# Kernel optimization log

Measured on AMD Instinct MI355X. Metric: run time of the kernel, lower is better.

## Reference

```python
import jax, jax.numpy as jnp
import numpy as np

H = 128  # hidden size

def _lstm_layer(x, Wih, Whh, bih, bhh):
    # x: [B, T, D]; Wih: [4H, D]; Whh: [4H, H]; biases: [4H]
    B, T, _ = x.shape
    # Precompute input contribution for all timesteps (one big GEMM)
    xg = jnp.einsum('btd,gd->btg', x, Wih) + bih + bhh  # [B, T, 4H]
    xg = jnp.swapaxes(xg, 0, 1)  # time-major [T, B, 4H]

    def step(carry, xt):
        h, c = carry
        gates = xt + h @ Whh.T  # [B, 4H]
        i, f, g, o = jnp.split(gates, 4, axis=-1)
        i = jax.nn.sigmoid(i)
        f = jax.nn.sigmoid(f)
        g = jnp.tanh(g)
        o = jax.nn.sigmoid(o)
        c = f * c + i * g
        h = o * jnp.tanh(c)
        return (h, c), h

    h0 = jnp.zeros((B, H), dtype=x.dtype)
    c0 = jnp.zeros((B, H), dtype=x.dtype)
    (_, _), hs = jax.lax.scan(step, (h0, c0), xg)
    return jnp.swapaxes(hs, 0, 1)  # [B, T, H]


def setup_inputs() -> dict:
    key = jax.random.key(0)
    ks = jax.random.split(key, 9)
    B, T, D = 32, 2048, 64
    s0 = 1.0 / np.sqrt(H)
    x = jax.random.normal(ks[0], (B, T, D), dtype=jnp.float32)
    # layer 0: input dim 64, layer 1: input dim 128 (torch gate order i,f,g,o)
    Wih0 = jax.random.uniform(ks[1], (4 * H, D), jnp.float32, -s0, s0)
    Whh0 = jax.random.uniform(ks[2], (4 * H, H), jnp.float32, -s0, s0)
    bih0 = jax.random.uniform(ks[3], (4 * H,), jnp.float32, -s0, s0)
    bhh0 = jax.random.uniform(ks[4], (4 * H,), jnp.float32, -s0, s0)
    Wih1 = jax.random.uniform(ks[5], (4 * H, H), jnp.float32, -s0, s0)
    Whh1 = jax.random.uniform(ks[6], (4 * H, H), jnp.float32, -s0, s0)
    bih1 = jax.random.uniform(ks[7], (4 * H,), jnp.float32, -s0, s0)
    bhh1 = jax.random.uniform(ks[8], (4 * H,), jnp.float32, -s0, s0)
    return {"x": x, "Wih0": Wih0, "Whh0": Whh0, "bih0": bih0, "bhh0": bhh0,
            "Wih1": Wih1, "Whh1": Whh1, "bih1": bih1, "bhh1": bhh1}


def reference(x, Wih0, Whh0, bih0, bhh0, Wih1, Whh1, bih1, bhh1):
    h = _lstm_layer(x, Wih0, Whh0, bih0, bhh0)
    h = _lstm_layer(h, Wih1, Whh1, bih1, bhh1)
    return h  # [B, T, H] full hidden-state sequence of the top layer
```

## Files before the change

### kernel.cpp

```cpp
#include <hip/hip_runtime.h>

#define TLEN 2048
#define BATCH 32
#define DIN 64
#define HID 128
#define RING 256
#define CHK 8

typedef _Float16 h2 __attribute__((ext_vector_type(2)));
typedef float f4 __attribute__((ext_vector_type(4)));
typedef unsigned int u32;

#if defined(__has_builtin)
#if __has_builtin(__builtin_amdgcn_fdot2)
#define FDOT2(a, b, c) __builtin_amdgcn_fdot2((a), (b), (c), false)
#endif
#endif
#ifndef FDOT2
#define FDOT2(a, b, c) ((c) + (float)(a).x * (float)(b).x + (float)(a).y * (float)(b).y)
#endif
#define DOT2U(wu, hv, acc) FDOT2(__builtin_bit_cast(h2, (wu)), (hv), (acc))

__device__ __forceinline__ float sigm(float x) { return 1.0f / (1.0f + __expf(-x)); }
__device__ __forceinline__ float tanh_c(float x) {
    x = fminf(fmaxf(x, -15.0f), 15.0f);
    float e = __expf(2.0f * x);
    return (e - 1.0f) / (e + 1.0f);
}
__device__ __forceinline__ void qreduce(float (&v)[4]) {
    #pragma unroll
    for (int m = 0; m < 4; ++m) {
        v[m] += __shfl_xor(v[m], 1, 4);
        v[m] += __shfl_xor(v[m], 2, 4);
    }
}

__device__ __forceinline__ u32 aload_rlx(u32* p) {
    return __hip_atomic_load(p, __ATOMIC_RELAXED, __HIP_MEMORY_SCOPE_AGENT);
}
__device__ __forceinline__ u32 aload_acq(u32* p) {
    return __hip_atomic_load(p, __ATOMIC_ACQUIRE, __HIP_MEMORY_SCOPE_AGENT);
}
__device__ __forceinline__ void astore_rlx(u32* p, u32 v) {
    __hip_atomic_store(p, v, __ATOMIC_RELAXED, __HIP_MEMORY_SCOPE_AGENT);
}
__device__ __forceinline__ void astore_rel(u32* p, u32 v) {
    __hip_atomic_store(p, v, __ATOMIC_RELEASE, __HIP_MEMORY_SCOPE_AGENT);
}

__device__ __forceinline__ void load_w_slice(const float* __restrict__ W,
                                             int rg, int kg, u32 (&w)[64]) {
    #pragma unroll
    for (int m = 0; m < 4; ++m) {
        const float2* a = (const float2*)(W + (size_t)(rg + 128 * m) * HID + kg * 32);
        #pragma unroll
        for (int i = 0; i < 16; ++i) {
            float2 v = a[i];
            h2 x; x.x = (_Float16)v.x; x.y = (_Float16)v.y;
            w[m * 16 + i] = __builtin_bit_cast(u32, x);
        }
    }
    #pragma unroll
    for (int i = 0; i < 64; ++i) asm volatile("" : "+v"(w[i]));
}
__device__ __forceinline__ void dot_slice(const u32 (&w)[64],
                                          const uint4* __restrict__ H,
                                          float (&p)[4]) {
    #pragma unroll
    for (int qr = 0; qr < 4; ++qr) {
        u32 hw[4];
        *(uint4*)hw = H[qr];
        #pragma unroll
        for (int ww = 0; ww < 4; ++ww) {
            const h2 hv = __builtin_bit_cast(h2, hw[ww]);
            #pragma unroll
            for (int m = 0; m < 4; ++m)
                p[m] = DOT2U(w[m * 16 + qr * 4 + ww], hv, p[m]);
        }
    }
}

__global__ __launch_bounds__(512) void xg_precompute(
    const float* __restrict__ X, const float* __restrict__ Wih0,
    const float* __restrict__ bih0, const float* __restrict__ bhh0,
    _Float16* __restrict__ XG)
{
    __shared__ float xs[16][DIN];
    const int blk = blockIdx.x;
    const int b   = blk / (TLEN / 16);
    const int tc  = blk % (TLEN / 16);
    const int j   = threadIdx.x;
    const int row = (j >> 2) + 128 * (j & 3);

    const float* xsrc = X + ((size_t)b * TLEN + (size_t)tc * 16) * DIN;
    for (int i = j; i < 16 * DIN; i += 512) ((float*)xs)[i] = xsrc[i];
    __syncthreads();

    f4 w[16];
    const f4* wp = (const f4*)(Wih0 + (size_t)row * DIN);
    #pragma unroll
    for (int i = 0; i < 16; ++i) w[i] = wp[i];
    const float bias = bih0[row] + bhh0[row];

    _Float16* dst = XG + ((size_t)b * TLEN + (size_t)tc * 16) * 512 + j;
    #pragma unroll 4
    for (int t = 0; t < 16; ++t) {
        float acc = bias;
        const f4* xv = (const f4*)&xs[t][0];
        #pragma unroll
        for (int i = 0; i < 16; ++i) {
            f4 x4 = xv[i];
            acc += w[i][0] * x4[0] + w[i][1] * x4[1] + w[i][2] * x4[2] + w[i][3] * x4[3];
        }
        dst[(size_t)t * 512] = (_Float16)acc;
    }
}

__global__ __launch_bounds__(512, 2) void lstm2_pipe(
    const _Float16* __restrict__ XG0,
    const float* __restrict__ Whh0,
    const float* __restrict__ Wih1, const float* __restrict__ Whh1,
    const float* __restrict__ bih1, const float* __restrict__ bhh1,
    float* __restrict__ Out,
    u32* __restrict__ H0g,
    u32* __restrict__ XG1,
    u32* __restrict__ Flags)
{
    const int role = blockIdx.x / BATCH;
    const int b    = blockIdx.x % BATCH;
    const int t0   = threadIdx.x;
    const int rg   = t0 >> 2;
    const int kg   = t0 & 3;

    u32* F0 = Flags + (size_t)b * 16;
    u32* F1 = Flags + (size_t)(32 + b) * 16;
    u32* C2 = Flags + (size_t)(64 + b) * 16;

    if (role == 0) {
        __shared__ alignas(16) _Float16 hl[2][HID];
        u32 w[64];
        load_w_slice(Whh0, rg, kg, w);
        if (t0 < HID) { hl[0][t0] = (_Float16)0.0f; hl[1][t0] = (_Float16)0.0f; }
        float c0 = 0.0f;
        const _Float16* xgp = XG0 + (size_t)b * TLEN * 512 + t0;
        u32* h0out = H0g + (size_t)b * TLEN * 64;
        _Float16 xga = xgp[0];
        _Float16 xgb = xgp[512];
        __syncthreads();

        for (int t = 0; t < TLEN; ++t) {
            const int cur = t & 1, prv = cur ^ 1;
            const float xgv = (float)xga;
            xga = xgb;
            { int tn = (t + 2 < TLEN) ? t + 2 : TLEN - 1; xgb = xgp[(size_t)tn * 512]; }

            float p[4];
            #pragma unroll
            for (int m = 0; m < 4; ++m) p[m] = (kg == m) ? xgv : 0.0f;
            dot_slice(w, (const uint4*)&hl[prv][kg * 32], p);
            qreduce(p);
            float ii = sigm(p[0]), ff = sigm(p[1]);
            float gg = tanh_c(p[2]), oo = sigm(p[3]);
            c0 = ff * c0 + ii * gg;
            if (kg == 0) hl[cur][rg] = (_Float16)(oo * tanh_c(c0));
            __syncthreads();
            if (t0 < 64)
                astore_rlx(&h0out[(size_t)t * 64 + t0], ((const u32*)hl[cur])[t0]);
            if (t0 == 0 && (t & (CHK - 1)) == (CHK - 1))
                astore_rel(F0, (u32)(t + 1));
        }
    } else if (role == 1) {
        __shared__ alignas(16) u32 h0c[CHK * 64];
        u32 w[64];
        load_w_slice(Wih1, rg, kg, w);
        const int rowk = rg + 128 * kg;
        const float B1 = bih1[rowk] + bhh1[rowk];
        u32* H0in = H0g + (size_t)b * TLEN * 64;
        u32* xout = XG1 + (size_t)b * RING * 512;
        u32 sc = 0;
        __syncthreads();

        for (int c = 0; c < TLEN / CHK; ++c) {
            const int tbase = c * CHK;
            if (t0 == 0) {
                u32 av; long g = 0;
                do { av = aload_acq(F0);
                     if (av >= (u32)(tbase + CHK)) break;
                     __builtin_amdgcn_s_sleep(2);
                } while (++g < 50000000L);
                if (tbase + CHK > (int)sc + (RING - 64)) {
                    g = 0;
                    do { sc = aload_rlx(C2);
                         if (tbase + CHK <= (int)sc + (RING - 64)) break;
                         __builtin_amdgcn_s_sleep(2);
                    } while (++g < 50000000L);
                }
            }
            __syncthreads();
            h0c[t0] = aload_rlx(&H0in[(size_t)tbase * 64 + t0]);
            __syncthreads();

            #pragma unroll
            for (int s = 0; s < CHK; ++s) {
                const int t = tbase + s;
                float p[4];
                #pragma unroll
                for (int m = 0; m < 4; ++m) p[m] = (kg == m) ? B1 : 0.0f;
                dot_slice(w, (const uint4*)&h0c[s * 64 + kg * 16], p);
                qreduce(p);
                astore_rlx(&xout[(size_t)((t & (RING - 1))) * 512 + t0],
                           __builtin_bit_cast(u32, p[kg]));
            }
            asm volatile("s_waitcnt vmcnt(0)" ::: "memory");
            __syncthreads();
            if (t0 == 0) astore_rel(F1, (u32)(tbase + CHK));
        }
    } else {
        __shared__ alignas(16) _Float16 hl[2][HID];
        __shared__ alignas(16) u32 xgc[CHK * 512];
        u32 w[64];
        load_w_slice(Whh1, rg, kg, w);
        if (t0 < HID) { hl[0][t0] = (_Float16)0.0f; hl[1][t0] = (_Float16)0.0f; }
        u32* xin = XG1 + (size_t)b * RING * 512;
        float c1 = 0.0f;
        __syncthreads();

        for (int c = 0; c < TLEN / CHK; ++c) {
            const int tbase = c * CHK;
            if (t0 == 0) {
                u32 av; long g = 0;
                do { av = aload_acq(F1);
                     if (av >= (u32)(tbase + CHK)) break;
                     __builtin_amdgcn_s_sleep(2);
                } while (++g < 50000000L);
            }
            __syncthreads();
            const size_t rbase = (size_t)(tbase & (RING - 1)) * 512;
            #pragma unroll
            for (int k = 0; k < CHK; ++k)
                xgc[k * 512 + t0] = aload_rlx(&xin[rbase + k * 512 + t0]);
            __syncthreads();

            #pragma unroll 1
            for (int s = 0; s < CHK; ++s) {
                const int t = tbase + s;
                const int cur = t & 1, prv = cur ^ 1;
                const float xgv = __builtin_bit_cast(float, xgc[s * 512 + t0]);

                float q[4];
                #pragma unroll
                for (int m = 0; m < 4; ++m) q[m] = (kg == m) ? xgv : 0.0f;
                dot_slice(w, (const uint4*)&hl[prv][kg * 32], q);
                qreduce(q);
                float ii = sigm(q[0]), ff = sigm(q[1]);
                float gg = tanh_c(q[2]), oo = sigm(q[3]);
                c1 = ff * c1 + ii * gg;
                float h1v = oo * tanh_c(c1);
                if (kg == 0) {
                    hl[cur][rg] = (_Float16)h1v;
                    Out[((size_t)b * TLEN + t) * HID + rg] = h1v;
                }
                __syncthreads();
            }
            if (t0 == 0 && (c & 3) == 3)
                astore_rlx(C2, (u32)(tbase + CHK));
        }
    }
}

__global__ __launch_bounds__(512, 2) void lstm2_persist(
    const float* __restrict__ X,
    const float* __restrict__ Wih0, const float* __restrict__ Whh0,
    const float* __restrict__ bih0, const float* __restrict__ bhh0,
    const float* __restrict__ Wih1, const float* __restrict__ Whh1,
    const float* __restrict__ bih1, const float* __restrict__ bhh1,
    float* __restrict__ Out)
{
    __shared__ unsigned int wih0_lds[512 * 33];
    __shared__ _Float16 h0buf[2][HID];
    __shared__ _Float16 h1buf[2][HID];

    const int b  = blockIdx.x;
    const int t  = threadIdx.x;
    const int rg = t >> 2;
    const int kg = t & 3;

    {
        const float2* src = (const float2*)(Wih0 + t * DIN);
        #pragma unroll
        for (int i = 0; i < 32; ++i) {
            float2 v = src[i];
            h2 p; p.x = (_Float16)v.x; p.y = (_Float16)v.y;
            wih0_lds[t * 33 + i] = __builtin_bit_cast(unsigned int, p);
        }
    }
    if (t < HID) {
        h0buf[0][t] = (_Float16)0.0f; h0buf[1][t] = (_Float16)0.0f;
        h1buf[0][t] = (_Float16)0.0f; h1buf[1][t] = (_Float16)0.0f;
    }

    h2 whh0[4][16], wih1[4][16], whh1[4][16];
    float bi0[4], bi1[4];
    #pragma unroll
    for (int m = 0; m < 4; ++m) {
        const int row = rg + 128 * m;
        const float2* a = (const float2*)(Whh0 + row * HID + kg * 32);
        const float2* c = (const float2*)(Wih1 + row * HID + kg * 32);
        const float2* d = (const float2*)(Whh1 + row * HID + kg * 32);
        #pragma unroll
        for (int i = 0; i < 16; ++i) {
            float2 v; h2 w;
            v = a[i]; w.x = (_Float16)v.x; w.y = (_Float16)v.y; whh0[m][i] = w;
            v = c[i]; w.x = (_Float16)v.x; w.y = (_Float16)v.y; wih1[m][i] = w;
            v = d[i]; w.x = (_Float16)v.x; w.y = (_Float16)v.y; whh1[m][i] = w;
        }
        bi0[m] = (kg == 0) ? (bih0[row] + bhh0[row]) : 0.0f;
        bi1[m] = (kg == 0) ? (bih1[row] + bhh1[row]) : 0.0f;
    }

    float c0 = 0.0f, c1 = 0.0f;
    __syncthreads();

    f4 xA[4], xB[4];
    {
        const f4* xp = (const f4*)(X + ((size_t)b * TLEN) * DIN + kg * 16);
        #pragma unroll
        for (int j = 0; j < 4; ++j) xA[j] = xp[j];
    }

    auto step = [&](int tt, f4 (&xc)[4], f4 (&xn)[4]) {
        const int cur = tt & 1, nxt = cur ^ 1;
        h2 xh[8];
        const float* xf = (const float*)xc;
        #pragma unroll
        for (int j = 0; j < 8; ++j) {
            h2 p; p.x = (_Float16)xf[2 * j]; p.y = (_Float16)xf[2 * j + 1];
            xh[j] = p;
        }
        {
            const int tn = (tt + 1 < TLEN) ? tt + 1 : TLEN - 1;
            const f4* xp = (const f4*)(X + ((size_t)b * TLEN + tn) * DIN + kg * 16);
            #pragma unroll
            for (int j = 0; j < 4; ++j) xn[j] = xp[j];
        }
        float p0[4];
        #pragma unroll
        for (int m = 0; m < 4; ++m) p0[m] = bi0[m];
        #pragma unroll
        for (int m = 0; m < 4; ++m) {
            const unsigned int* wr = &wih0_lds[(rg + 128 * m) * 33 + kg * 8];
            #pragma unroll
            for (int i = 0; i < 8; ++i) {
                h2 w = __builtin_bit_cast(h2, wr[i]);
                p0[m] = FDOT2(w, xh[i], p0[m]);
            }
        }
        {
            const unsigned int* hr = (const unsigned int*)&h0buf[cur][0];
            #pragma unroll
            for (int i = 0; i < 16; ++i) {
                h2 hv = __builtin_bit_cast(h2, hr[kg * 16 + i]);
                #pragma unroll
                for (int m = 0; m < 4; ++m)
                    p0[m] = FDOT2(whh0[m][i], hv, p0[m]);
            }
        }
        #pragma unroll
        for (int m = 0; m < 4; ++m) {
            p0[m] += __shfl_xor(p0[m], 1, 4);
            p0[m] += __shfl_xor(p0[m], 2, 4);
        }
        {
            float ii = sigm(p0[0]), ff = sigm(p0[1]);
            float gg = tanh_c(p0[2]), oo = sigm(p0[3]);
            c0 = ff * c0 + ii * gg;
            float h0v = oo * tanh_c(c0);
            if (kg == 0) h0buf[nxt][rg] = (_Float16)h0v;
        }
        __syncthreads();
        float q[4];
        #pragma unroll
        for (int m = 0; m < 4; ++m) q[m] = bi1[m];
        {
            const unsigned int* hr = (const unsigned int*)&h0buf[nxt][0];
            #pragma unroll
            for (int i = 0; i < 16; ++i) {
                h2 hv = __builtin_bit_cast(h2, hr[kg * 16 + i]);
                #pragma unroll
                for (int m = 0; m < 4; ++m)
                    q[m] = FDOT2(wih1[m][i], hv, q[m]);
            }
        }
        {
            const unsigned int* hr = (const unsigned int*)&h1buf[cur][0];
            #pragma unroll
            for (int i = 0; i < 16; ++i) {
                h2 hv = __builtin_bit_cast(h2, hr[kg * 16 + i]);
                #pragma unroll
                for (int m = 0; m < 4; ++m)
                    q[m] = FDOT2(whh1[m][i], hv, q[m]);
            }
        }
        #pragma unroll
        for (int m = 0; m < 4; ++m) {
            q[m] += __shfl_xor(q[m], 1, 4);
            q[m] += __shfl_xor(q[m], 2, 4);
        }
        {
            float ii = sigm(q[0]), ff = sigm(q[1]);
            float gg = tanh_c(q[2]), oo = sigm(q[3]);
            c1 = ff * c1 + ii * gg;
            float h1v = oo * tanh_c(c1);
            if (kg == 0) {
                h1buf[nxt][rg] = (_Float16)h1v;
                Out[((size_t)b * TLEN + tt) * HID + rg] = h1v;
            }
        }
        __syncthreads();
    };

    for (int tt = 0; tt < TLEN; tt += 2) {
        step(tt, xA, xB);
        step(tt + 1, xB, xA);
    }
}

extern "C" void kernel_launch(void* const* d_in, const int* in_sizes, int n_in,
                              void* d_out, int out_size, void* d_ws, size_t ws_size,
                              hipStream_t stream) {
    const float* X    = (const float*)d_in[0];
    const float* Wih0 = (const float*)d_in[1];
    const float* Whh0 = (const float*)d_in[2];
    const float* bih0 = (const float*)d_in[3];
    const float* bhh0 = (const float*)d_in[4];
    const float* Wih1 = (const float*)d_in[5];
    const float* Whh1 = (const float*)d_in[6];
    const float* bih1 = (const float*)d_in[7];
    const float* bhh1 = (const float*)d_in[8];
    float* Out = (float*)d_out;

    const size_t XG0_B  = (size_t)BATCH * TLEN * 512 * 2;
    const size_t H0_B   = (size_t)BATCH * TLEN * 64 * 4;
    const size_t XG1_B  = (size_t)BATCH * RING * 512 * 4;
    const size_t FLAG_B = 96 * 16 * 4;
    const size_t NEED   = XG0_B + H0_B + XG1_B + FLAG_B;

    if (ws_size >= NEED) {
        char* ws = (char*)d_ws;
        _Float16* XG0 = (_Float16*)ws;
        u32* H0g   = (u32*)(ws + XG0_B);
        u32* XG1   = (u32*)(ws + XG0_B + H0_B);
        u32* Flags = (u32*)(ws + XG0_B + H0_B + XG1_B);

        hipMemsetAsync(Flags, 0, FLAG_B, stream);
        xg_precompute<<<dim3(BATCH * (TLEN / 16)), dim3(512), 0, stream>>>(
            X, Wih0, bih0, bhh0, XG0);
        lstm2_pipe<<<dim3(3 * BATCH), dim3(512), 0, stream>>>(
            XG0, Whh0, Wih1, Whh1, bih1, bhh1, Out, H0g, XG1, Flags);
    } else {
        lstm2_persist<<<dim3(BATCH), dim3(512), 0, stream>>>(
            X, Wih0, Whh0, bih0, bhh0, Wih1, Whh1, bih1, bhh1, Out);
    }
}
```

Baseline: 2.338 ms.

## Split LSTM recurrence dot products across eight lanes with 1024-thread blocks

The pipelined two-layer LSTM kernel now runs 1024 threads per block instead of 512. Each gate row's 128-wide dot product is split across eight lanes instead of four, so each thread holds half as many fp16 weight registers and does half as many fdot2 operations per timestep. The aim is to shorten the per-step serial latency of the recurrence. In exchange it adds a third shuffle-reduction stage, has redundant lanes (only four of the eight lanes carry gate values), and makes each per-step barrier span twice as many waves.

New measurement: 2.921 ms. 24.9% more time.

```diff
diff --git a/kernel.cpp b/kernel.cpp
--- a/kernel.cpp
+++ b/kernel.cpp
@@ -27,11 +27,12 @@
     float e = __expf(2.0f * x);
     return (e - 1.0f) / (e + 1.0f);
 }
-__device__ __forceinline__ void qreduce(float (&v)[4]) {
+__device__ __forceinline__ void qreduce8(float (&v)[4]) {
     #pragma unroll
     for (int m = 0; m < 4; ++m) {
-        v[m] += __shfl_xor(v[m], 1, 4);
-        v[m] += __shfl_xor(v[m], 2, 4);
+        v[m] += __shfl_xor(v[m], 1, 8);
+        v[m] += __shfl_xor(v[m], 2, 8);
+        v[m] += __shfl_xor(v[m], 4, 8);
     }
 }
 
@@ -48,26 +49,26 @@
     __hip_atomic_store(p, v, __ATOMIC_RELEASE, __HIP_MEMORY_SCOPE_AGENT);
 }
 
-__device__ __forceinline__ void load_w_slice(const float* __restrict__ W,
-                                             int rg, int kg, u32 (&w)[64]) {
+__device__ __forceinline__ void load_w8(const float* __restrict__ W,
+                                        int rg, int kg, u32 (&w)[32]) {
     #pragma unroll
     for (int m = 0; m < 4; ++m) {
-        const float2* a = (const float2*)(W + (size_t)(rg + 128 * m) * HID + kg * 32);
-        #pragma unroll
-        for (int i = 0; i < 16; ++i) {
+        const float2* a = (const float2*)(W + (size_t)(rg + 128 * m) * HID + kg * 16);
+        #pragma unroll
+        for (int i = 0; i < 8; ++i) {
             float2 v = a[i];
             h2 x; x.x = (_Float16)v.x; x.y = (_Float16)v.y;
-            w[m * 16 + i] = __builtin_bit_cast(u32, x);
-        }
-    }
-    #pragma unroll
-    for (int i = 0; i < 64; ++i) asm volatile("" : "+v"(w[i]));
-}
-__device__ __forceinline__ void dot_slice(const u32 (&w)[64],
-                                          const uint4* __restrict__ H,
-                                          float (&p)[4]) {
-    #pragma unroll
-    for (int qr = 0; qr < 4; ++qr) {
+            w[m * 8 + i] = __builtin_bit_cast(u32, x);
+        }
+    }
+    #pragma unroll
+    for (int i = 0; i < 32; ++i) asm volatile("" : "+v"(w[i]));
+}
+__device__ __forceinline__ void dot8(const u32 (&w)[32],
+                                     const uint4* __restrict__ H,
+                                     float (&p)[4]) {
+    #pragma unroll
+    for (int qr = 0; qr < 2; ++qr) {
         u32 hw[4];
         *(uint4*)hw = H[qr];
         #pragma unroll
@@ -75,7 +76,7 @@
             const h2 hv = __builtin_bit_cast(h2, hw[ww]);
             #pragma unroll
             for (int m = 0; m < 4; ++m)
-                p[m] = DOT2U(w[m * 16 + qr * 4 + ww], hv, p[m]);
+                p[m] = DOT2U(w[m * 8 + qr * 4 + ww], hv, p[m]);
         }
     }
 }
@@ -116,7 +117,7 @@
     }
 }
 
-__global__ __launch_bounds__(512, 2) void lstm2_pipe(
+__global__ __launch_bounds__(1024, 1) void lstm2_pipe(
     const _Float16* __restrict__ XG0,
     const float* __restrict__ Whh0,
     const float* __restrict__ Wih1, const float* __restrict__ Whh1,
@@ -129,8 +130,9 @@
     const int role = blockIdx.x / BATCH;
     const int b    = blockIdx.x % BATCH;
     const int t0   = threadIdx.x;
-    const int rg   = t0 >> 2;
-    const int kg   = t0 & 3;
+    const int rg   = t0 >> 3;
+    const int kg   = t0 & 7;
+    const int g    = kg & 3;
 
     u32* F0 = Flags + (size_t)b * 16;
     u32* F1 = Flags + (size_t)(32 + b) * 16;
@@ -138,11 +140,11 @@
 
     if (role == 0) {
         __shared__ alignas(16) _Float16 hl[2][HID];
-        u32 w[64];
-        load_w_slice(Whh0, rg, kg, w);
+        u32 w[32];
+        load_w8(Whh0, rg, kg, w);
         if (t0 < HID) { hl[0][t0] = (_Float16)0.0f; hl[1][t0] = (_Float16)0.0f; }
         float c0 = 0.0f;
-        const _Float16* xgp = XG0 + (size_t)b * TLEN * 512 + t0;
+        const _Float16* xgp = XG0 + (size_t)b * TLEN * 512 + rg * 4 + g;
         u32* h0out = H0g + (size_t)b * TLEN * 64;
         _Float16 xga = xgp[0];
         _Float16 xgb = xgp[512];
@@ -157,8 +159,8 @@
             float p[4];
             #pragma unroll
             for (int m = 0; m < 4; ++m) p[m] = (kg == m) ? xgv : 0.0f;
-            dot_slice(w, (const uint4*)&hl[prv][kg * 32], p);
-            qreduce(p);
+            dot8(w, (const uint4*)&hl[prv][kg * 16], p);
+            qreduce8(p);
             float ii = sigm(p[0]), ff = sigm(p[1]);
             float gg = tanh_c(p[2]), oo = sigm(p[3]);
             c0 = ff * c0 + ii * gg;
@@ -171,9 +173,9 @@
         }
     } else if (role == 1) {
         __shared__ alignas(16) u32 h0c[CHK * 64];
-        u32 w[64];
-        load_w_slice(Wih1, rg, kg, w);
-        const int rowk = rg + 128 * kg;
+        u32 w[32];
+        load_w8(Wih1, rg, kg, w);
+        const int rowk = rg + 128 * g;
         const float B1 = bih1[rowk] + bhh1[rowk];
         u32* H0in = H0g + (size_t)b * TLEN * 64;
         u32* xout = XG1 + (size_t)b * RING * 512;
@@ -183,21 +185,22 @@
         for (int c = 0; c < TLEN / CHK; ++c) {
             const int tbase = c * CHK;
             if (t0 == 0) {
-                u32 av; long g = 0;
+                u32 av; long gd = 0;
                 do { av = aload_acq(F0);
                      if (av >= (u32)(tbase + CHK)) break;
                      __builtin_amdgcn_s_sleep(2);
-                } while (++g < 50000000L);
+                } while (++gd < 50000000L);
                 if (tbase + CHK > (int)sc + (RING - 64)) {
-                    g = 0;
+                    gd = 0;
                     do { sc = aload_rlx(C2);
                          if (tbase + CHK <= (int)sc + (RING - 64)) break;
                          __builtin_amdgcn_s_sleep(2);
-                    } while (++g < 50000000L);
+                    } while (++gd < 50000000L);
                 }
             }
             __syncthreads();
-            h0c[t0] = aload_rlx(&H0in[(size_t)tbase * 64 + t0]);
+            if (t0 < CHK * 64)
+                h0c[t0] = aload_rlx(&H0in[(size_t)tbase * 64 + t0]);
             __syncthreads();
 
             #pragma unroll
@@ -206,10 +209,11 @@
                 float p[4];
                 #pragma unroll
                 for (int m = 0; m < 4; ++m) p[m] = (kg == m) ? B1 : 0.0f;
-                dot_slice(w, (const uint4*)&h0c[s * 64 + kg * 16], p);
-                qreduce(p);
-                astore_rlx(&xout[(size_t)((t & (RING - 1))) * 512 + t0],
-                           __builtin_bit_cast(u32, p[kg]));
+                dot8(w, (const uint4*)&h0c[s * 64 + kg * 8], p);
+                qreduce8(p);
+                if (kg < 4)
+                    astore_rlx(&xout[(size_t)(t & (RING - 1)) * 512 + rg * 4 + kg],
+                               __builtin_bit_cast(u32, p[kg]));
             }
             asm volatile("s_waitcnt vmcnt(0)" ::: "memory");
             __syncthreads();
@@ -218,8 +222,8 @@
     } else {
         __shared__ alignas(16) _Float16 hl[2][HID];
         __shared__ alignas(16) u32 xgc[CHK * 512];
-        u32 w[64];
-        load_w_slice(Whh1, rg, kg, w);
+        u32 w[32];
+        load_w8(Whh1, rg, kg, w);
         if (t0 < HID) { hl[0][t0] = (_Float16)0.0f; hl[1][t0] = (_Float16)0.0f; }
         u32* xin = XG1 + (size_t)b * RING * 512;
         float c1 = 0.0f;
@@ -228,30 +232,31 @@
         for (int c = 0; c < TLEN / CHK; ++c) {
             const int tbase = c * CHK;
             if (t0 == 0) {
-                u32 av; long g = 0;
+                u32 av; long gd = 0;
                 do { av = aload_acq(F1);
                      if (av >= (u32)(tbase + CHK)) break;
                      __builtin_amdgcn_s_sleep(2);
-                } while (++g < 50000000L);
+                } while (++gd < 50000000L);
             }
             __syncthreads();
             const size_t rbase = (size_t)(tbase & (RING - 1)) * 512;
             #pragma unroll
-            for (int k = 0; k < CHK; ++k)
-                xgc[k * 512 + t0] = aload_rlx(&xin[rbase + k * 512 + t0]);
+            for (int k = 0; k < (CHK * 512) / 1024; ++k)
+                xgc[k * 1024 + t0] = aload_rlx(&xin[rbase + k * 1024 + t0]);
             __syncthreads();
 
             #pragma unroll 1
             for (int s = 0; s < CHK; ++s) {
                 const int t = tbase + s;
                 const int cur = t & 1, prv = cur ^ 1;
-                const float xgv = __builtin_bit_cast(float, xgc[s * 512 + t0]);
+                const float xgv = __builtin_bit_cast(float,
+                                    xgc[s * 512 + rg * 4 + g]);
 
                 float q[4];
                 #pragma unroll
                 for (int m = 0; m < 4; ++m) q[m] = (kg == m) ? xgv : 0.0f;
-                dot_slice(w, (const uint4*)&hl[prv][kg * 32], q);
-                qreduce(q);
+                dot8(w, (const uint4*)&hl[prv][kg * 16], q);
+                qreduce8(q);
                 float ii = sigm(q[0]), ff = sigm(q[1]);
                 float gg = tanh_c(q[2]), oo = sigm(q[3]);
                 c1 = ff * c1 + ii * gg;
@@ -455,7 +460,7 @@
         hipMemsetAsync(Flags, 0, FLAG_B, stream);
         xg_precompute<<<dim3(BATCH * (TLEN / 16)), dim3(512), 0, stream>>>(
             X, Wih0, bih0, bhh0, XG0);
-        lstm2_pipe<<<dim3(3 * BATCH), dim3(512), 0, stream>>>(
+        lstm2_pipe<<<dim3(3 * BATCH), dim3(1024), 0, stream>>>(
             XG0, Whh0, Wih1, Whh1, bih1, bhh1, Out, H0g, XG1, Flags);
     } else {
         lstm2_persist<<<dim3(BATCH), dim3(512), 0, stream>>>(
```

## Stage recurrent weights in LDS and use exp2/rcp gate activations

Applied to the files above, without the earlier changes.

Each role of the pipelined LSTM kernel now converts its 512x128 weight matrix to fp16 once and stores it in a padded shared-memory pool. The matvec reads weights from there every step instead of keeping a 64-register slice per thread, and the launch bound no longer asks for two blocks per CU. The aim is to cut register pressure and possible spills. The trade-off is extra LDS reads on the serial critical path of every timestep. Sigmoid and tanh are rewritten with the hardware exp2 and reciprocal builtins to shorten the activation latency.

Measured after the change: 2.160 ms. 1.08x faster.

```diff
diff --git a/kernel.cpp b/kernel.cpp
--- a/kernel.cpp
+++ b/kernel.cpp
@@ -6,7 +6,9 @@
 #define HID 128
 #define RING 256
 #define CHK 8
-
+#define WRS 68
+
+typedef _Float16 f16;
 typedef _Float16 h2 __attribute__((ext_vector_type(2)));
 typedef float f4 __attribute__((ext_vector_type(4)));
 typedef unsigned int u32;
@@ -21,11 +23,28 @@
 #endif
 #define DOT2U(wu, hv, acc) FDOT2(__builtin_bit_cast(h2, (wu)), (hv), (acc))
 
-__device__ __forceinline__ float sigm(float x) { return 1.0f / (1.0f + __expf(-x)); }
+#if defined(__has_builtin)
+#if __has_builtin(__builtin_amdgcn_exp2f)
+#define FEXP2(x) __builtin_amdgcn_exp2f(x)
+#endif
+#if __has_builtin(__builtin_amdgcn_rcpf)
+#define FRCP(x) __builtin_amdgcn_rcpf(x)
+#endif
+#endif
+#ifndef FEXP2
+#define FEXP2(x) __expf((x) * 0.69314718f)
+#endif
+#ifndef FRCP
+#define FRCP(x) (1.0f / (x))
+#endif
+
+__device__ __forceinline__ float sigm(float x) {
+    return FRCP(1.0f + FEXP2(-1.44269504f * x));
+}
 __device__ __forceinline__ float tanh_c(float x) {
     x = fminf(fmaxf(x, -15.0f), 15.0f);
-    float e = __expf(2.0f * x);
-    return (e - 1.0f) / (e + 1.0f);
+    float e = FEXP2(2.88539008f * x);
+    return (e - 1.0f) * FRCP(e + 1.0f);
 }
 __device__ __forceinline__ void qreduce(float (&v)[4]) {
     #pragma unroll
@@ -35,10 +54,10 @@
     }
 }
 
-__device__ __forceinline__ u32 aload_rlx(u32* p) {
+__device__ __forceinline__ u32 aload_rlx(const u32* p) {
     return __hip_atomic_load(p, __ATOMIC_RELAXED, __HIP_MEMORY_SCOPE_AGENT);
 }
-__device__ __forceinline__ u32 aload_acq(u32* p) {
+__device__ __forceinline__ u32 aload_acq(const u32* p) {
     return __hip_atomic_load(p, __ATOMIC_ACQUIRE, __HIP_MEMORY_SCOPE_AGENT);
 }
 __device__ __forceinline__ void astore_rlx(u32* p, u32 v) {
@@ -48,34 +67,35 @@
     __hip_atomic_store(p, v, __ATOMIC_RELEASE, __HIP_MEMORY_SCOPE_AGENT);
 }
 
-__device__ __forceinline__ void load_w_slice(const float* __restrict__ W,
-                                             int rg, int kg, u32 (&w)[64]) {
+__device__ __forceinline__ void stage_weights(const float* __restrict__ W,
+                                              u32* __restrict__ wl, int t0) {
+    const float2* src2 = (const float2*)W;
+    for (int idx = t0; idx < 512 * 64; idx += 512) {
+        const int row = idx >> 6, d = idx & 63;
+        float2 v = src2[(size_t)row * 64 + d];
+        h2 x; x.x = (f16)v.x; x.y = (f16)v.y;
+        wl[(size_t)row * WRS + d] = __builtin_bit_cast(u32, x);
+    }
+}
+
+__device__ __forceinline__ void dot_wlds(const u32* __restrict__ wl,
+                                         int rg, int kg,
+                                         const u32* __restrict__ hsl,
+                                         float (&p)[4]) {
+    uint4 hq[4];
+    #pragma unroll
+    for (int i4 = 0; i4 < 4; ++i4) hq[i4] = *(const uint4*)&hsl[i4 * 4];
     #pragma unroll
     for (int m = 0; m < 4; ++m) {
-        const float2* a = (const float2*)(W + (size_t)(rg + 128 * m) * HID + kg * 32);
-        #pragma unroll
-        for (int i = 0; i < 16; ++i) {
-            float2 v = a[i];
-            h2 x; x.x = (_Float16)v.x; x.y = (_Float16)v.y;
-            w[m * 16 + i] = __builtin_bit_cast(u32, x);
-        }
-    }
-    #pragma unroll
-    for (int i = 0; i < 64; ++i) asm volatile("" : "+v"(w[i]));
-}
-__device__ __forceinline__ void dot_slice(const u32 (&w)[64],
-                                          const uint4* __restrict__ H,
-                                          float (&p)[4]) {
-    #pragma unroll
-    for (int qr = 0; qr < 4; ++qr) {
-        u32 hw[4];
-        *(uint4*)hw = H[qr];
-        #pragma unroll
-        for (int ww = 0; ww < 4; ++ww) {
-            const h2 hv = __builtin_bit_cast(h2, hw[ww]);
-            #pragma unroll
-            for (int m = 0; m < 4; ++m)
-                p[m] = DOT2U(w[m * 16 + qr * 4 + ww], hv, p[m]);
+        const u32* wb = wl + (size_t)(rg + 128 * m) * WRS + kg * 16;
+        #pragma unroll
+        for (int i4 = 0; i4 < 4; ++i4) {
+            const uint4 wq = *(const uint4*)&wb[i4 * 4];
+            const u32* hw = (const u32*)&hq[i4];
+            p[m] = DOT2U(wq.x, __builtin_bit_cast(h2, hw[0]), p[m]);
+            p[m] = DOT2U(wq.y, __builtin_bit_cast(h2, hw[1]), p[m]);
+            p[m] = DOT2U(wq.z, __builtin_bit_cast(h2, hw[2]), p[m]);
+            p[m] = DOT2U(wq.w, __builtin_bit_cast(h2, hw[3]), p[m]);
         }
     }
 }
@@ -83,7 +103,7 @@
 __global__ __launch_bounds__(512) void xg_precompute(
     const float* __restrict__ X, const float* __restrict__ Wih0,
     const float* __restrict__ bih0, const float* __restrict__ bhh0,
-    _Float16* __restrict__ XG)
+    f16* __restrict__ XG)
 {
     __shared__ float xs[16][DIN];
     const int blk = blockIdx.x;
@@ -102,7 +122,7 @@
     for (int i = 0; i < 16; ++i) w[i] = wp[i];
     const float bias = bih0[row] + bhh0[row];
 
-    _Float16* dst = XG + ((size_t)b * TLEN + (size_t)tc * 16) * 512 + j;
+    f16* dst = XG + ((size_t)b * TLEN + (size_t)tc * 16) * 512 + j;
     #pragma unroll 4
     for (int t = 0; t < 16; ++t) {
         float acc = bias;
@@ -112,12 +132,12 @@
             f4 x4 = xv[i];
             acc += w[i][0] * x4[0] + w[i][1] * x4[1] + w[i][2] * x4[2] + w[i][3] * x4[3];
         }
-        dst[(size_t)t * 512] = (_Float16)acc;
-    }
-}
-
-__global__ __launch_bounds__(512, 2) void lstm2_pipe(
-    const _Float16* __restrict__ XG0,
+        dst[(size_t)t * 512] = (f16)acc;
+    }
+}
+
+__global__ __launch_bounds__(512) void lstm2_pipe(
+    const f16* __restrict__ XG0,
     const float* __restrict__ Whh0,
     const float* __restrict__ Wih1, const float* __restrict__ Whh1,
     const float* __restrict__ bih1, const float* __restrict__ bhh1,
@@ -126,6 +146,8 @@
     u32* __restrict__ XG1,
     u32* __restrict__ Flags)
 {
+    __shared__ alignas(16) u32 pool[39040];
+
     const int role = blockIdx.x / BATCH;
     const int b    = blockIdx.x % BATCH;
     const int t0   = threadIdx.x;
@@ -137,15 +159,14 @@
     u32* C2 = Flags + (size_t)(64 + b) * 16;
 
     if (role == 0) {
-        __shared__ alignas(16) _Float16 hl[2][HID];
-        u32 w[64];
-        load_w_slice(Whh0, rg, kg, w);
-        if (t0 < HID) { hl[0][t0] = (_Float16)0.0f; hl[1][t0] = (_Float16)0.0f; }
+        stage_weights(Whh0, pool, t0);
+        u32* hl = pool + 34816;
+        if (t0 < 128) hl[t0] = 0u;
         float c0 = 0.0f;
-        const _Float16* xgp = XG0 + (size_t)b * TLEN * 512 + t0;
+        const f16* xgp = XG0 + (size_t)b * TLEN * 512 + t0;
         u32* h0out = H0g + (size_t)b * TLEN * 64;
-        _Float16 xga = xgp[0];
-        _Float16 xgb = xgp[512];
+        f16 xga = xgp[0];
+        f16 xgb = xgp[512];
         __syncthreads();
 
         for (int t = 0; t < TLEN; ++t) {
@@ -157,22 +178,25 @@
             float p[4];
             #pragma unroll
             for (int m = 0; m < 4; ++m) p[m] = (kg == m) ? xgv : 0.0f;
-            dot_slice(w, (const uint4*)&hl[prv][kg * 32], p);
+            dot_wlds(pool, rg, kg, hl + prv * 64 + kg * 16, p);
             qreduce(p);
             float ii = sigm(p[0]), ff = sigm(p[1]);
             float gg = tanh_c(p[2]), oo = sigm(p[3]);
             c0 = ff * c0 + ii * gg;
-            if (kg == 0) hl[cur][rg] = (_Float16)(oo * tanh_c(c0));
+            if (kg == 0) {
+                h2 hv2; hv2.x = (f16)(oo * tanh_c(c0)); hv2.y = hv2.x;
+                f16* hf = (f16*)(hl + cur * 64);
+                hf[rg] = hv2.x;
+            }
             __syncthreads();
             if (t0 < 64)
-                astore_rlx(&h0out[(size_t)t * 64 + t0], ((const u32*)hl[cur])[t0]);
+                astore_rlx(&h0out[(size_t)t * 64 + t0], hl[cur * 64 + t0]);
             if (t0 == 0 && (t & (CHK - 1)) == (CHK - 1))
                 astore_rel(F0, (u32)(t + 1));
         }
     } else if (role == 1) {
-        __shared__ alignas(16) u32 h0c[CHK * 64];
-        u32 w[64];
-        load_w_slice(Wih1, rg, kg, w);
+        stage_weights(Wih1, pool, t0);
+        u32* h0c = pool + 34816;
         const int rowk = rg + 128 * kg;
         const float B1 = bih1[rowk] + bhh1[rowk];
         u32* H0in = H0g + (size_t)b * TLEN * 64;
@@ -206,9 +230,9 @@
                 float p[4];
                 #pragma unroll
                 for (int m = 0; m < 4; ++m) p[m] = (kg == m) ? B1 : 0.0f;
-                dot_slice(w, (const uint4*)&h0c[s * 64 + kg * 16], p);
+                dot_wlds(pool, rg, kg, h0c + s * 64 + kg * 16, p);
                 qreduce(p);
-                astore_rlx(&xout[(size_t)((t & (RING - 1))) * 512 + t0],
+                astore_rlx(&xout[(size_t)(t & (RING - 1)) * 512 + t0],
                            __builtin_bit_cast(u32, p[kg]));
             }
             asm volatile("s_waitcnt vmcnt(0)" ::: "memory");
@@ -216,11 +240,10 @@
             if (t0 == 0) astore_rel(F1, (u32)(tbase + CHK));
         }
     } else {
-        __shared__ alignas(16) _Float16 hl[2][HID];
-        __shared__ alignas(16) u32 xgc[CHK * 512];
-        u32 w[64];
-        load_w_slice(Whh1, rg, kg, w);
-        if (t0 < HID) { hl[0][t0] = (_Float16)0.0f; hl[1][t0] = (_Float16)0.0f; }
+        stage_weights(Whh1, pool, t0);
+        u32* xgc = pool + 34816;
+        u32* hl  = pool + 38912;
+        if (t0 < 128) hl[t0] = 0u;
         u32* xin = XG1 + (size_t)b * RING * 512;
         float c1 = 0.0f;
         __syncthreads();
@@ -250,14 +273,15 @@
                 float q[4];
                 #pragma unroll
                 for (int m = 0; m < 4; ++m) q[m] = (kg == m) ? xgv : 0.0f;
-                dot_slice(w, (const uint4*)&hl[prv][kg * 32], q);
+                dot_wlds(pool, rg, kg, hl + prv * 64 + kg * 16, q);
                 qreduce(q);
                 float ii = sigm(q[0]), ff = sigm(q[1]);
                 float gg = tanh_c(q[2]), oo = sigm(q[3]);
                 c1 = ff * c1 + ii * gg;
                 float h1v = oo * tanh_c(c1);
                 if (kg == 0) {
-                    hl[cur][rg] = (_Float16)h1v;
+                    f16* hf = (f16*)(hl + cur * 64);
+                    hf[rg] = (f16)h1v;
                     Out[((size_t)b * TLEN + t) * HID + rg] = h1v;
                 }
                 __syncthreads();
@@ -277,8 +301,8 @@
     float* __restrict__ Out)
 {
     __shared__ unsigned int wih0_lds[512 * 33];
-    __shared__ _Float16 h0buf[2][HID];
-    __shared__ _Float16 h1buf[2][HID];
+    __shared__ f16 h0buf[2][HID];
+    __shared__ f16 h1buf[2][HID];
 
     const int b  = blockIdx.x;
     const int t  = threadIdx.x;
@@ -290,13 +314,13 @@
         #pragma unroll
         for (int i = 0; i < 32; ++i) {
             float2 v = src[i];
-            h2 p; p.x = (_Float16)v.x; p.y = (_Float16)v.y;
+            h2 p; p.x = (f16)v.x; p.y = (f16)v.y;
             wih0_lds[t * 33 + i] = __builtin_bit_cast(unsigned int, p);
         }
     }
     if (t < HID) {
-        h0buf[0][t] = (_Float16)0.0f; h0buf[1][t] = (_Float16)0.0f;
-        h1buf[0][t] = (_Float16)0.0f; h1buf[1][t] = (_Float16)0.0f;
+        h0buf[0][t] = (f16)0.0f; h0buf[1][t] = (f16)0.0f;
+        h1buf[0][t] = (f16)0.0f; h1buf[1][t] = (f16)0.0f;
     }
 
     h2 whh0[4][16], wih1[4][16], whh1[4][16];
@@ -310,9 +334,9 @@
         #pragma unroll
         for (int i = 0; i < 16; ++i) {
             float2 v; h2 w;
-            v = a[i]; w.x = (_Float16)v.x; w.y = (_Float16)v.y; whh0[m][i] = w;
-            v = c[i]; w.x = (_Float16)v.x; w.y = (_Float16)v.y; wih1[m][i] = w;
-            v = d[i]; w.x = (_Float16)v.x; w.y = (_Float16)v.y; whh1[m][i] = w;
+            v = a[i]; w.x = (f16)v.x; w.y = (f16)v.y; whh0[m][i] = w;
+            v = c[i]; w.x = (f16)v.x; w.y = (f16)v.y; wih1[m][i] = w;
+            v = d[i]; w.x = (f16)v.x; w.y = (f16)v.y; whh1[m][i] = w;
         }
         bi0[m] = (kg == 0) ? (bih0[row] + bhh0[row]) : 0.0f;
         bi1[m] = (kg == 0) ? (bih1[row] + bhh1[row]) : 0.0f;
@@ -334,7 +358,7 @@
         const float* xf = (const float*)xc;
         #pragma unroll
         for (int j = 0; j < 8; ++j) {
-            h2 p; p.x = (_Float16)xf[2 * j]; p.y = (_Float16)xf[2 * j + 1];
+            h2 p; p.x = (f16)xf[2 * j]; p.y = (f16)xf[2 * j + 1];
             xh[j] = p;
         }
         {
@@ -365,17 +389,13 @@
                     p0[m] = FDOT2(whh0[m][i], hv, p0[m]);
             }
         }
-        #pragma unroll
-        for (int m = 0; m < 4; ++m) {
-            p0[m] += __shfl_xor(p0[m], 1, 4);
-            p0[m] += __shfl_xor(p0[m], 2, 4);
-        }
+        qreduce(p0);
         {
             float ii = sigm(p0[0]), ff = sigm(p0[1]);
             float gg = tanh_c(p0[2]), oo = sigm(p0[3]);
             c0 = ff * c0 + ii * gg;
             float h0v = oo * tanh_c(c0);
-            if (kg == 0) h0buf[nxt][rg] = (_Float16)h0v;
+            if (kg == 0) h0buf[nxt][rg] = (f16)h0v;
         }
         __syncthreads();
         float q[4];
@@ -401,18 +421,14 @@
                     q[m] = FDOT2(whh1[m][i], hv, q[m]);
             }
         }
-        #pragma unroll
-        for (int m = 0; m < 4; ++m) {
-            q[m] += __shfl_xor(q[m], 1, 4);
-            q[m] += __shfl_xor(q[m], 2, 4);
-        }
+        qreduce(q);
         {
             float ii = sigm(q[0]), ff = sigm(q[1]);
             float gg = tanh_c(q[2]), oo = sigm(q[3]);
             c1 = ff * c1 + ii * gg;
             float h1v = oo * tanh_c(c1);
             if (kg == 0) {
-                h1buf[nxt][rg] = (_Float16)h1v;
+                h1buf[nxt][rg] = (f16)h1v;
                 Out[((size_t)b * TLEN + tt) * HID + rg] = h1v;
             }
         }
@@ -447,7 +463,7 @@
 
     if (ws_size >= NEED) {
         char* ws = (char*)d_ws;
-        _Float16* XG0 = (_Float16*)ws;
+        f16* XG0   = (f16*)ws;
         u32* H0g   = (u32*)(ws + XG0_B);
         u32* XG1   = (u32*)(ws + XG0_B + H0_B);
         u32* Flags = (u32*)(ws + XG0_B + H0_B + XG1_B);
```
